# Optimization experiments

Measured on AMD Instinct MI355X. Metric: run time of the kernel, lower is better.

Reference implementation:

```python
import jax, jax.numpy as jnp
import numpy as np

EPS = 1e-6
NUM_HEADS = 16

def rmsnorm(x, w):
    # x: [..., d], w: [d]
    norm = jax.lax.rsqrt(jnp.mean(x * x, axis=-1, keepdims=True) + EPS)
    return w * (x * norm)

def setup_inputs() -> dict:
    key = jax.random.key(0)
    ks = jax.random.split(key, 6)
    B, N, C = 2, 2048, 1024
    H = NUM_HEADS
    hd = C // H
    x = jax.random.normal(ks[0], (B, N, C), dtype=jnp.float32)
    scale = 1.0 / np.sqrt(C)
    qkv_w = jax.random.normal(ks[1], (C, 3 * C), dtype=jnp.float32) * scale
    qkv_b = jnp.zeros((3 * C,), dtype=jnp.float32)
    q_norm_w = jnp.ones((hd,), dtype=jnp.float32)
    k_norm_w = jnp.ones((hd,), dtype=jnp.float32)
    proj_w = jax.random.normal(ks[2], (C, C), dtype=jnp.float32) * scale
    proj_b = jnp.zeros((C,), dtype=jnp.float32)
    return {"x": x, "qkv_w": qkv_w, "qkv_b": qkv_b,
            "q_norm_w": q_norm_w, "k_norm_w": k_norm_w,
            "proj_w": proj_w, "proj_b": proj_b}

def reference(x, qkv_w, qkv_b, q_norm_w, k_norm_w, proj_w, proj_b):
    B, N, C = x.shape
    H = NUM_HEADS
    hd = C // H
    qkv = x @ qkv_w + qkv_b                       # [B,N,3C]
    qkv = qkv.reshape(B, N, 3, H, hd)
    q, k, v = qkv[:, :, 0], qkv[:, :, 1], qkv[:, :, 2]  # [B,N,H,hd]
    q = jnp.transpose(q, (0, 2, 1, 3))            # [B,H,N,hd]
    k = jnp.transpose(k, (0, 2, 1, 3))
    v = jnp.transpose(v, (0, 2, 1, 3))
    q = rmsnorm(q, q_norm_w)
    k = rmsnorm(k, k_norm_w)
    scores = jnp.einsum('bhqd,bhkd->bhqk', q, k) / jnp.sqrt(jnp.float32(hd))
    attn = jax.nn.softmax(scores, axis=-1)
    out = jnp.einsum('bhqk,bhkd->bhqd', attn, v)  # [B,H,N,hd]
    out = jnp.transpose(out, (0, 2, 1, 3)).reshape(B, N, C)
    return out @ proj_w + proj_b
```

## Files before the change

### kernel.cpp

```cpp
#include <hip/hip_runtime.h>

typedef unsigned short u16;
typedef unsigned int u32;
typedef __bf16 bf16x8 __attribute__((ext_vector_type(8)));
typedef float f32x4 __attribute__((ext_vector_type(4)));
typedef unsigned short u16x8 __attribute__((ext_vector_type(8)));
typedef unsigned short u16x4 __attribute__((ext_vector_type(4)));

__device__ __forceinline__ float bf2f(u16 u) {
    union { unsigned int i; float f; } c; c.i = ((unsigned int)u) << 16; return c.f;
}
__device__ __forceinline__ u16 f2bf(float f) {
    union { float f; unsigned int i; } c; c.f = f;
    unsigned int r = c.i + 0x7FFFu + ((c.i >> 16) & 1u);
    return (u16)(r >> 16);
}
__device__ __forceinline__ u16 f2bf_rtz(float f) {
    union { float f; unsigned int i; } c; c.f = f;
    return (u16)(c.i >> 16);
}
__device__ __forceinline__ float fast_exp2(float x) {
#if __has_builtin(__builtin_amdgcn_exp2f)
    return __builtin_amdgcn_exp2f(x);
#else
    return exp2f(x);
#endif
}
__device__ __forceinline__ void async16(const void* g, void* l) {
    __builtin_amdgcn_global_load_lds(
        (const __attribute__((address_space(1))) u32*)g,
        (__attribute__((address_space(3))) u32*)l, 16, 0, 0);
}

__global__ __launch_bounds__(256) void prep(
    const float* __restrict__ X, u16* __restrict__ Xb,
    const float* __restrict__ qkv_w, u16* __restrict__ qwT,
    const float* __restrict__ proj_w, u16* __restrict__ pwT)
{
    __shared__ float tile[32][33];
    const int blk = blockIdx.x;
    const int t = threadIdx.x;
    if (blk < 2048) {
        const size_t i = ((size_t)blk * 256 + t) * 8;
        u16x8 h;
        #pragma unroll
        for (int e = 0; e < 8; ++e) h[e] = f2bf(X[i + e]);
        *(u16x8*)&Xb[i] = h;
        return;
    }
    const float* W; u16* Th; int K, N, bx, by;
    if (blk < 5120) {
        W = qkv_w; Th = qwT; K = 1024; N = 3072;
        bx = (blk - 2048) % 96; by = (blk - 2048) / 96;
    } else {
        W = proj_w; Th = pwT; K = 1024; N = 1024;
        bx = (blk - 5120) % 32; by = (blk - 5120) / 32;
    }
    const int bk = by * 32, bn = bx * 32;
    const int tx = t & 31, ty = t >> 5;
    #pragma unroll
    for (int r = ty; r < 32; r += 8)
        tile[r][tx] = W[(size_t)(bk + r) * N + bn + tx];
    __syncthreads();
    #pragma unroll
    for (int r = ty; r < 32; r += 8)
        Th[(size_t)(bn + r) * K + bk + tx] = f2bf(tile[tx][r]);
}

__global__ __launch_bounds__(256) void gemm_qkv(
    const u16* __restrict__ AH, const u16* __restrict__ BH,
    const float* __restrict__ bias,
    u16* __restrict__ Qb, u16* __restrict__ Kb, u16* __restrict__ Vt,
    const float* __restrict__ qw, const float* __restrict__ kw)
{
    const int K = 1024;
    __shared__ __align__(16) u16 AhT[128 * 32];
    __shared__ __align__(16) u16 BhT[128 * 32];
    const int t = threadIdx.x;
    const int bm = blockIdx.y * 128, bn = blockIdx.x * 128;
    const int wave = t >> 6, lane = t & 63;
    const int wm = (wave >> 1) * 64, wn = (wave & 1) * 64;
    const int l15 = lane & 15, quad = lane >> 4;
    const int srow = lane >> 2, scol = (lane & 3) * 8;

    f32x4 acc[4][4];
    const f32x4 zero = {0.0f, 0.0f, 0.0f, 0.0f};
    #pragma unroll
    for (int i = 0; i < 4; ++i)
        #pragma unroll
        for (int j = 0; j < 4; ++j) acc[i][j] = zero;

    for (int k0 = 0; k0 < K; k0 += 32) {
        #pragma unroll
        for (int rr = 0; rr < 2; ++rr) {
            const int r0 = (rr * 4 + wave) * 16;
            const size_t ga = (size_t)(bm + r0 + srow) * K + k0 + scol;
            const size_t gb = (size_t)(bn + r0 + srow) * K + k0 + scol;
            async16(&AH[ga], &AhT[r0 * 32]);
            async16(&BH[gb], &BhT[r0 * 32]);
        }
        __syncthreads();
        bf16x8 ah[4], bh[4];
        #pragma unroll
        for (int i = 0; i < 4; ++i)
            ah[i] = *(const bf16x8*)&AhT[(wm + i * 16 + l15) * 32 + quad * 8];
        #pragma unroll
        for (int j = 0; j < 4; ++j)
            bh[j] = *(const bf16x8*)&BhT[(wn + j * 16 + l15) * 32 + quad * 8];
        #pragma unroll
        for (int i = 0; i < 4; ++i)
            #pragma unroll
            for (int j = 0; j < 4; ++j)
                acc[i][j] = __builtin_amdgcn_mfma_f32_16x16x32_bf16(
                    ah[i], bh[j], acc[i][j], 0, 0, 0);
        __syncthreads();
    }

    const int gc0 = bn + wn;
    const int sec = gc0 >> 10;
    const int h = (gc0 & 1023) >> 6;
    const int b = bm >> 11;
    const int bhd = b * 16 + h;
    float bv[4], wj[4];
    #pragma unroll
    for (int j = 0; j < 4; ++j) {
        const int d = j * 16 + l15;
        bv[j] = bias[gc0 + d];
        wj[j] = (sec == 2) ? 0.0f : (sec ? kw[d] : qw[d] * 0.18033688011f);
    }
    if (sec < 2) {
        u16* dst = sec ? Kb : Qb;
        #pragma unroll
        for (int i = 0; i < 4; ++i) {
            float val[4][4];
            float ss[4] = {0.0f, 0.0f, 0.0f, 0.0f};
            #pragma unroll
            for (int j = 0; j < 4; ++j)
                #pragma unroll
                for (int r = 0; r < 4; ++r) {
                    val[j][r] = acc[i][j][r] + bv[j];
                    ss[r] += val[j][r] * val[j][r];
                }
            #pragma unroll
            for (int r = 0; r < 4; ++r) {
                #pragma unroll
                for (int m = 1; m < 16; m <<= 1)
                    ss[r] += __shfl_xor(ss[r], m, 64);
                const float nrm = rsqrtf(ss[r] * 0.015625f + 1e-6f);
                const int n = (bm + wm + i * 16 + quad * 4 + r) & 2047;
                const size_t rowb = ((size_t)bhd * 2048 + n) * 64;
                #pragma unroll
                for (int j = 0; j < 4; ++j)
                    dst[rowb + j * 16 + l15] = f2bf(val[j][r] * nrm * wj[j]);
            }
        }
    } else {
        #pragma unroll
        for (int i = 0; i < 4; ++i) {
            const int n0 = (bm + wm + i * 16 + quad * 4) & 2047;
            #pragma unroll
            for (int j = 0; j < 4; ++j) {
                const int d = j * 16 + l15;
                u16x4 pk;
                #pragma unroll
                for (int r = 0; r < 4; ++r)
                    pk[r] = f2bf(acc[i][j][r] + bv[j]);
                *(u16x4*)&Vt[((size_t)bhd * 64 + d) * 2048 + n0] = pk;
            }
        }
    }
}

__global__ __launch_bounds__(256) void gemm_proj(
    const u16* __restrict__ AH, const u16* __restrict__ BH,
    const float* __restrict__ bias, float* __restrict__ C)
{
    const int N = 1024, K = 1024;
    __shared__ __align__(16) u16 AhT[64 * 32];
    __shared__ __align__(16) u16 BhT[128 * 32];
    const int t = threadIdx.x;
    const int bm = blockIdx.y * 64, bn = blockIdx.x * 128;
    const int wave = t >> 6, lane = t & 63;
    const int l15 = lane & 15, quad = lane >> 4;
    const int srow = lane >> 2, scol = (lane & 3) * 8;

    f32x4 acc[4][2];
    const f32x4 zero = {0.0f, 0.0f, 0.0f, 0.0f};
    #pragma unroll
    for (int i = 0; i < 4; ++i)
        #pragma unroll
        for (int j = 0; j < 2; ++j) acc[i][j] = zero;

    for (int k0 = 0; k0 < K; k0 += 32) {
        {
            const int r0 = wave * 16;
            async16(&AH[(size_t)(bm + r0 + srow) * K + k0 + scol],
                    &AhT[r0 * 32]);
        }
        #pragma unroll
        for (int cc = 0; cc < 2; ++cc) {
            const int r0 = (wave * 2 + cc) * 16;
            async16(&BH[(size_t)(bn + r0 + srow) * K + k0 + scol],
                    &BhT[r0 * 32]);
        }
        __syncthreads();
        bf16x8 ah[4], bh[2];
        #pragma unroll
        for (int i = 0; i < 4; ++i)
            ah[i] = *(const bf16x8*)&AhT[(i * 16 + l15) * 32 + quad * 8];
        #pragma unroll
        for (int j = 0; j < 2; ++j)
            bh[j] = *(const bf16x8*)
                &BhT[(wave * 32 + j * 16 + l15) * 32 + quad * 8];
        #pragma unroll
        for (int i = 0; i < 4; ++i)
            #pragma unroll
            for (int j = 0; j < 2; ++j)
                acc[i][j] = __builtin_amdgcn_mfma_f32_16x16x32_bf16(
                    ah[i], bh[j], acc[i][j], 0, 0, 0);
        __syncthreads();
    }

    #pragma unroll
    for (int j = 0; j < 2; ++j) {
        const int col = bn + wave * 32 + j * 16 + l15;
        const float bv = bias[col];
        #pragma unroll
        for (int i = 0; i < 4; ++i) {
            const int row = bm + i * 16 + quad * 4;
            #pragma unroll
            for (int r = 0; r < 4; ++r)
                C[(size_t)(row + r) * N + col] = acc[i][j][r] + bv;
        }
    }
}

__global__ __launch_bounds__(256) void flash_attn_mfma(
    const u16* __restrict__ Qb, const u16* __restrict__ Kb,
    const u16* __restrict__ Vt, u16* __restrict__ Attn)
{
    __shared__ __align__(16) u16 Klds[2 * 64 * 64];
    __shared__ __align__(16) u16 Vlds[2 * 64 * 64];
    __shared__ __align__(16) u16 Plds[128][72];
    __shared__ float Lbuf[128];

    const int t = threadIdx.x;
    const int bid = blockIdx.x;
    const int bh = bid & 31;
    const int qt = bid >> 5;
    const int n0 = qt * 128;
    const size_t kbase = (size_t)bh * 2048 * 64;
    const size_t vbase = (size_t)bh * 64 * 2048;
    const int wave = t >> 6, lane = t & 63;
    const int l15 = lane & 15, quad = lane >> 4;
    const int srow8 = lane >> 3;
    const int sgrp = lane & 7;

    bf16x8 qf[2][2];
    #pragma unroll
    for (int qs = 0; qs < 2; ++qs) {
        const size_t qrow =
            ((size_t)bh * 2048 + n0 + wave * 32 + qs * 16 + l15) * 64;
        qf[qs][0] = *(const bf16x8*)&Qb[qrow + quad * 8];
        qf[qs][1] = *(const bf16x8*)&Qb[qrow + 32 + quad * 8];
    }

    int kofs[4][2];
    #pragma unroll
    for (int nt = 0; nt < 4; ++nt) {
        const int row = nt * 16 + l15;
        kofs[nt][0] = row * 64 + ((quad ^ (row & 7)) * 8);
        kofs[nt][1] = row * 64 + (((quad + 4) ^ (row & 7)) * 8);
    }

    f32x4 o[2][4];
    const f32x4 zero = {0.0f, 0.0f, 0.0f, 0.0f};
    #pragma unroll
    for (int qs = 0; qs < 2; ++qs)
        #pragma unroll
        for (int dt = 0; dt < 4; ++dt) o[qs][dt] = zero;
    float lsum[2] = {0.0f, 0.0f};

    #pragma unroll
    for (int cc = 0; cc < 2; ++cc) {
        const int r0 = (wave + cc * 4) * 8;
        const int row = r0 + srow8;
        const int gg = sgrp ^ (row & 7);
        async16(&Kb[kbase + (size_t)row * 64 + gg * 8], &Klds[r0 * 64]);
        async16(&Vt[vbase + (size_t)row * 2048 + gg * 8], &Vlds[r0 * 64]);
    }

    for (int kt = 0; kt < 32; ++kt) {
        __syncthreads();
        if (kt + 1 < 32) {
            const int nb = ((kt + 1) & 1) * 4096;
            #pragma unroll
            for (int cc = 0; cc < 2; ++cc) {
                const int r0 = (wave + cc * 4) * 8;
                const int row = r0 + srow8;
                const int gg = sgrp ^ (row & 7);
                async16(&Kb[kbase + (size_t)((kt + 1) * 64 + row) * 64 + gg * 8],
                        &Klds[nb + r0 * 64]);
                async16(&Vt[vbase + (size_t)row * 2048 + (kt + 1) * 64 + gg * 8],
                        &Vlds[nb + r0 * 64]);
            }
        }
        const int cb = (kt & 1) * 4096;

        f32x4 s[2][4];
        #pragma unroll
        for (int nt = 0; nt < 4; ++nt) {
            bf16x8 kf0 = *(const bf16x8*)&Klds[cb + kofs[nt][0]];
            bf16x8 kf1 = *(const bf16x8*)&Klds[cb + kofs[nt][1]];
            #pragma unroll
            for (int qs = 0; qs < 2; ++qs) {
                s[qs][nt] = zero;
                s[qs][nt] = __builtin_amdgcn_mfma_f32_16x16x32_bf16(
                    kf0, qf[qs][0], s[qs][nt], 0, 0, 0);
                s[qs][nt] = __builtin_amdgcn_mfma_f32_16x16x32_bf16(
                    kf1, qf[qs][1], s[qs][nt], 0, 0, 0);
            }
        }

        #pragma unroll
        for (int qs = 0; qs < 2; ++qs) {
            const int prow = wave * 32 + qs * 16 + l15;
            #pragma unroll
            for (int nt = 0; nt < 4; ++nt) {
                u16x4 pk;
                #pragma unroll
                for (int r = 0; r < 4; ++r) {
                    const float p = fast_exp2(s[qs][nt][r]);
                    lsum[qs] += p;
                    pk[r] = f2bf_rtz(p);
                }
                *(u16x4*)&Plds[prow][nt * 16 + quad * 4] = pk;
            }
        }

        bf16x8 pf[2][2];
        #pragma unroll
        for (int qs = 0; qs < 2; ++qs) {
            const int prow = wave * 32 + qs * 16 + l15;
            pf[qs][0] = *(const bf16x8*)&Plds[prow][quad * 8];
            pf[qs][1] = *(const bf16x8*)&Plds[prow][quad * 8 + 32];
        }

        #pragma unroll
        for (int dt = 0; dt < 4; ++dt) {
            bf16x8 vf0 = *(const bf16x8*)&Vlds[cb + kofs[dt][0]];
            bf16x8 vf1 = *(const bf16x8*)&Vlds[cb + kofs[dt][1]];
            #pragma unroll
            for (int qs = 0; qs < 2; ++qs) {
                o[qs][dt] = __builtin_amdgcn_mfma_f32_16x16x32_bf16(
                    pf[qs][0], vf0, o[qs][dt], 0, 0, 0);
                o[qs][dt] = __builtin_amdgcn_mfma_f32_16x16x32_bf16(
                    pf[qs][1], vf1, o[qs][dt], 0, 0, 0);
            }
        }
    }

    #pragma unroll
    for (int qs = 0; qs < 2; ++qs) {
        lsum[qs] += __shfl_xor(lsum[qs], 16, 64);
        lsum[qs] += __shfl_xor(lsum[qs], 32, 64);
        if (quad == 0) Lbuf[wave * 32 + qs * 16 + l15] = lsum[qs];
    }
    const size_t obase =
        ((size_t)(bh >> 4) * 2048 + n0) * 1024 + (bh & 15) * 64;
    #pragma unroll
    for (int qs = 0; qs < 2; ++qs)
        #pragma unroll
        for (int r = 0; r < 4; ++r) {
            const float inv =
                1.0f / Lbuf[wave * 32 + qs * 16 + quad * 4 + r];
            const size_t rbase =
                obase + (size_t)(wave * 32 + qs * 16 + quad * 4 + r) * 1024;
            #pragma unroll
            for (int dt = 0; dt < 4; ++dt)
                Attn[rbase + dt * 16 + l15] = f2bf(o[qs][dt][r] * inv);
        }
}

extern "C" void kernel_launch(void* const* d_in, const int* in_sizes, int n_in,
                              void* d_out, int out_size, void* d_ws, size_t ws_size,
                              hipStream_t stream)
{
    const float* x      = (const float*)d_in[0];
    const float* qkv_w  = (const float*)d_in[1];
    const float* qkv_b  = (const float*)d_in[2];
    const float* q_nw   = (const float*)d_in[3];
    const float* k_nw   = (const float*)d_in[4];
    const float* proj_w = (const float*)d_in[5];
    const float* proj_b = (const float*)d_in[6];
    float* out = (float*)d_out;

    char* ws = (char*)d_ws;
    u16* AttnB = (u16*)ws;
    u16* qwT   = (u16*)(ws + 8388608);
    u16* pwT   = (u16*)(ws + 14680064);
    u16* Xb    = (u16*)(ws + 16777216);
    u16* QbB   = (u16*)(ws + 25165824);
    u16* KbB   = (u16*)(ws + 33554432);
    u16* VtB   = (u16*)(ws + 41943040);
    (void)in_sizes; (void)n_in; (void)out_size;
    if (ws_size < 50331648u) return;

    prep<<<dim3(6144), 256, 0, stream>>>(x, Xb, qkv_w, qwT, proj_w, pwT);
    gemm_qkv<<<dim3(3072 / 128, 4096 / 128), 256, 0, stream>>>(
        Xb, qwT, qkv_b, QbB, KbB, VtB, q_nw, k_nw);
    flash_attn_mfma<<<dim3(512), 256, 0, stream>>>(QbB, KbB, VtB, AttnB);
    gemm_proj<<<dim3(1024 / 128, 4096 / 64), 256, 0, stream>>>(
        AttnB, pwT, proj_b, out);
}
```

Before: 191.3 us.

## Permute V layout so softmax probabilities feed PV MFMA directly from registers

Changes how the QKV kernel writes V^T: key positions within each 64-wide block are permuted so that the S accumulator layout from the QK MFMA lines up with the A-operand layout of the PV MFMA. The exponentiated probabilities are then packed in registers into bf16x8 fragments, which removes the P shared-memory buffer and its write/read round trip. It also wraps the MFMA groups in s_setprio to favour matrix issue across waves, and adds a barrier before reading Lbuf. This frees LDS and LDS bandwidth but depends on the producer and consumer permutations staying consistent.

```diff
diff --git a/kernel.cpp b/kernel.cpp
--- a/kernel.cpp
+++ b/kernel.cpp
@@ -25,6 +25,9 @@
 #else
     return exp2f(x);
 #endif
+}
+__device__ __forceinline__ bf16x8 u2b(u16x8 v) {
+    return __builtin_bit_cast(bf16x8, v);
 }
 __device__ __forceinline__ void async16(const void* g, void* l) {
     __builtin_amdgcn_global_load_lds(
@@ -155,9 +158,10 @@
             }
         }
     } else {
+        const int nb = (bm + wm) & 2047;
         #pragma unroll
         for (int i = 0; i < 4; ++i) {
-            const int n0 = (bm + wm + i * 16 + quad * 4) & 2047;
+            const int s0 = (i & 1) * 32 + quad * 8 + (i >> 1) * 4;
             #pragma unroll
             for (int j = 0; j < 4; ++j) {
                 const int d = j * 16 + l15;
@@ -165,7 +169,7 @@
                 #pragma unroll
                 for (int r = 0; r < 4; ++r)
                     pk[r] = f2bf(acc[i][j][r] + bv[j]);
-                *(u16x4*)&Vt[((size_t)bhd * 64 + d) * 2048 + n0] = pk;
+                *(u16x4*)&Vt[((size_t)bhd * 64 + d) * 2048 + nb + s0] = pk;
             }
         }
     }
@@ -241,7 +245,6 @@
 {
     __shared__ __align__(16) u16 Klds[2 * 64 * 64];
     __shared__ __align__(16) u16 Vlds[2 * 64 * 64];
-    __shared__ __align__(16) u16 Plds[128][72];
     __shared__ float Lbuf[128];
 
     const int t = threadIdx.x;
@@ -312,6 +315,7 @@
         for (int nt = 0; nt < 4; ++nt) {
             bf16x8 kf0 = *(const bf16x8*)&Klds[cb + kofs[nt][0]];
             bf16x8 kf1 = *(const bf16x8*)&Klds[cb + kofs[nt][1]];
+            __builtin_amdgcn_s_setprio(1);
             #pragma unroll
             for (int qs = 0; qs < 2; ++qs) {
                 s[qs][nt] = zero;
@@ -320,36 +324,33 @@
                 s[qs][nt] = __builtin_amdgcn_mfma_f32_16x16x32_bf16(
                     kf1, qf[qs][1], s[qs][nt], 0, 0, 0);
             }
-        }
-
+            __builtin_amdgcn_s_setprio(0);
+        }
+
+        bf16x8 pf[2][2];
         #pragma unroll
         for (int qs = 0; qs < 2; ++qs) {
-            const int prow = wave * 32 + qs * 16 + l15;
-            #pragma unroll
-            for (int nt = 0; nt < 4; ++nt) {
-                u16x4 pk;
+            #pragma unroll
+            for (int m = 0; m < 2; ++m) {
+                u16x8 pk;
                 #pragma unroll
                 for (int r = 0; r < 4; ++r) {
-                    const float p = fast_exp2(s[qs][nt][r]);
-                    lsum[qs] += p;
-                    pk[r] = f2bf_rtz(p);
+                    const float p0 = fast_exp2(s[qs][m][r]);
+                    lsum[qs] += p0;
+                    pk[r] = f2bf_rtz(p0);
+                    const float p1 = fast_exp2(s[qs][m + 2][r]);
+                    lsum[qs] += p1;
+                    pk[4 + r] = f2bf_rtz(p1);
                 }
-                *(u16x4*)&Plds[prow][nt * 16 + quad * 4] = pk;
-            }
-        }
-
-        bf16x8 pf[2][2];
-        #pragma unroll
-        for (int qs = 0; qs < 2; ++qs) {
-            const int prow = wave * 32 + qs * 16 + l15;
-            pf[qs][0] = *(const bf16x8*)&Plds[prow][quad * 8];
-            pf[qs][1] = *(const bf16x8*)&Plds[prow][quad * 8 + 32];
+                pf[qs][m] = u2b(pk);
+            }
         }
 
         #pragma unroll
         for (int dt = 0; dt < 4; ++dt) {
             bf16x8 vf0 = *(const bf16x8*)&Vlds[cb + kofs[dt][0]];
             bf16x8 vf1 = *(const bf16x8*)&Vlds[cb + kofs[dt][1]];
+            __builtin_amdgcn_s_setprio(1);
             #pragma unroll
             for (int qs = 0; qs < 2; ++qs) {
                 o[qs][dt] = __builtin_amdgcn_mfma_f32_16x16x32_bf16(
@@ -357,6 +358,7 @@
                 o[qs][dt] = __builtin_amdgcn_mfma_f32_16x16x32_bf16(
                     pf[qs][1], vf1, o[qs][dt], 0, 0, 0);
             }
+            __builtin_amdgcn_s_setprio(0);
         }
     }
 
@@ -366,6 +368,7 @@
         lsum[qs] += __shfl_xor(lsum[qs], 32, 64);
         if (quad == 0) Lbuf[wave * 32 + qs * 16 + l15] = lsum[qs];
     }
+    __syncthreads();
     const size_t obase =
         ((size_t)(bh >> 4) * 2048 + n0) * 1024 + (bh & 15) * 64;
     #pragma unroll
```

Measured after the change: 199.9 us. 1.04x slower.
